# Optimization experiments

Hardware: AMD Instinct MI355X
Metric: run time of the kernel (lower is better)

The kernel has to match this reference:

```python
import jax, jax.numpy as jnp
import numpy as np

N_HEAD = 16
NEG = -1e30  # finite stand-in for -inf; keeps softmax NaN-free


def setup_inputs() -> dict:
    key = jax.random.key(0)
    k1, k2, k3, k4, k5, k6 = jax.random.split(key, 6)
    B, T, C = 4, 2048, 1024
    x = jax.random.normal(k1, (B, T, C), dtype=jnp.float32)
    # realistic right-padding: True = padded position
    lengths = jax.random.randint(k2, (B,), T // 2, T + 1)  # at least half valid
    padding_mask = jnp.arange(T)[None, :] >= lengths[:, None]  # [B,T] bool
    s = 0.02
    W_attn = jax.random.normal(k3, (C, 3 * C), dtype=jnp.float32) * s
    b_attn = jnp.zeros((3 * C,), dtype=jnp.float32)
    W_proj = jax.random.normal(k4, (C, C), dtype=jnp.float32) * s
    b_proj = jnp.zeros((C,), dtype=jnp.float32)
    return {"x": x, "padding_mask": padding_mask, "W_attn": W_attn,
            "b_attn": b_attn, "W_proj": W_proj, "b_proj": b_proj}


def reference(x, padding_mask, W_attn, b_attn, W_proj, b_proj):
    B, T, C = x.shape
    H, D = N_HEAD, C // N_HEAD
    qkv = x @ W_attn + b_attn  # [B,T,3C]
    q, k, v = jnp.split(qkv, 3, axis=-1)
    q = q.reshape(B, T, H, D).transpose(0, 2, 1, 3)  # [B,H,T,D]
    k = k.reshape(B, T, H, D).transpose(0, 2, 1, 3)
    v = v.reshape(B, T, H, D).transpose(0, 2, 1, 3)
    att = jnp.einsum('bhqd,bhkd->bhqk', q, k) / jnp.sqrt(jnp.float32(D))
    causal = jnp.tril(jnp.ones((T, T), dtype=bool))  # [T,T]
    invalid = padding_mask[:, None, None, :] | ~causal[None, None]  # [B,1,T,T] key invalid
    att = jnp.where(invalid, NEG, att)
    att = jax.nn.softmax(att, axis=-1)
    # rows where every key is masked: torch softmax gives NaN -> nan_to_num(0)
    any_valid = jnp.any(~invalid, axis=-1, keepdims=True)  # [B,1,T,1]
    att = jnp.where(any_valid, att, 0.0)
    y = jnp.einsum('bhqk,bhkd->bhqd', att, v)  # [B,H,T,D]
    y = y.transpose(0, 2, 1, 3).reshape(B, T, C)
    y = y @ W_proj + b_proj
    y = jnp.where(padding_mask[:, :, None], 0.0, y)
    return y
```

## Files before the change

kernel.cpp:

```cpp
#include <hip/hip_runtime.h>
#include <stdint.h>

#define T_SEQ 2048
#define CDIM  1024
#define NH    16
#define DH    64
#define BATCH 4
#define MROWS (BATCH * T_SEQ)
#define N3    (3 * CDIM)
#define NEGBIG -1e30f

typedef unsigned short u16;
typedef __attribute__((ext_vector_type(8))) __bf16 bf16x8;
typedef __attribute__((ext_vector_type(4))) __bf16 bf16x4;
typedef __attribute__((ext_vector_type(8))) unsigned short u16x8;
typedef __attribute__((ext_vector_type(4))) float f32x4;
typedef __attribute__((ext_vector_type(16))) float f32x16;
typedef __attribute__((ext_vector_type(4))) unsigned int u32x4;

__device__ inline u16 f2bf(float f) {
  uint32_t u = __builtin_bit_cast(uint32_t, f);
  u += 0x7FFFu + ((u >> 16) & 1u);
  return (u16)(u >> 16);
}

__device__ inline void gld_lds16(const void* g, void* l) {
  __builtin_amdgcn_global_load_lds(
      (const __attribute__((address_space(1))) void*)g,
      (__attribute__((address_space(3))) void*)l, 16, 0, 0);
}


__global__ __launch_bounds__(256) void cvt_f32_bf16(
    const float* __restrict__ in, u16* __restrict__ out, int n) {
  int i = (blockIdx.x * 256 + threadIdx.x) * 4;
  if (i >= n) return;
  float4 v = *(const float4*)&in[i];
  ushort4 o; o.x = f2bf(v.x); o.y = f2bf(v.y); o.z = f2bf(v.z); o.w = f2bf(v.w);
  *(ushort4*)&out[i] = o;
}

__global__ __launch_bounds__(256) void wt_tiled(
    const float* __restrict__ W, u16* __restrict__ WT, int K, int N) {
  __shared__ float tile[64][65];
  const int k0 = blockIdx.y * 64, n0 = blockIdx.x * 64;
  const int t = threadIdx.x, cr = t >> 6, cc = t & 63;
#pragma unroll
  for (int i = 0; i < 16; i++) {
    int r = i * 4 + cr;
    tile[r][cc] = W[(size_t)(k0 + r) * N + n0 + cc];
  }
  __syncthreads();
#pragma unroll
  for (int i = 0; i < 16; i++) {
    int r = i * 4 + cr;
    WT[(size_t)(n0 + r) * K + k0 + cc] = f2bf(tile[cc][r]);
  }
}

__global__ __launch_bounds__(256) void len_kernel(
    const void* __restrict__ maskp, int* __restrict__ lengths) {
  __shared__ int flag;
  __shared__ int red[256];
  const int t = threadIdx.x, b = blockIdx.x;
  if (t == 0) flag = 0;
  __syncthreads();
  const uint32_t* mw = (const uint32_t*)maskp;
  int f = 0;
  for (int i = t; i < 2048; i += 256) f |= (mw[i] > 1u) ? 1 : 0;
  if (f) atomicOr(&flag, 1);
  __syncthreads();
  int cnt = 0;
  if (flag) {
    const uint8_t* mb = (const uint8_t*)maskp;
    for (int i = t; i < T_SEQ; i += 256) cnt += (mb[(size_t)b * T_SEQ + i] == 0);
  } else {
    const int* mi = (const int*)maskp;
    for (int i = t; i < T_SEQ; i += 256) cnt += (mi[(size_t)b * T_SEQ + i] == 0);
  }
  red[t] = cnt;
  __syncthreads();
  for (int s = 128; s > 0; s >>= 1) {
    if (t < s) red[t] += red[t + s];
    __syncthreads();
  }
  if (t == 0) lengths[b] = red[0];
}

template <int MODE>
__global__ __launch_bounds__(256, 2) void gemm_bf16(
    const u16* __restrict__ A, const u16* __restrict__ Bt,
    const float* __restrict__ bias,
    u16* __restrict__ Qb, u16* __restrict__ Kb, u16* __restrict__ Vt,
    float* __restrict__ Out, const int* __restrict__ lengths,
    int Mdim, int Ndim, int Kdim) {
  __shared__ u16 SM[16384];
  u16* As = SM;
  u16* Bs = SM + 8192;
  const int t = threadIdx.x;
  const int lane = t & 63, wid = t >> 6;
  const int wr = wid >> 1, wc = wid & 1;
  const int r16 = lane & 15, kg = lane >> 4;
  const int m0 = blockIdx.y * 128, n0 = blockIdx.x * 128;
  const int bb = m0 >> 11, tt0 = m0 & 2047;

  if (tt0 >= lengths[bb]) {
    if (MODE == 1) {
      const float4 z4 = make_float4(0.f, 0.f, 0.f, 0.f);
#pragma unroll
      for (int i = 0; i < 16; i++) {
        int u = i * 256 + t;
        int r = u >> 5, c4 = u & 31;
        *(float4*)&Out[(size_t)(m0 + r) * CDIM + n0 + c4 * 4] = z4;
      }
    }
    return;
  }

  f32x4 acc[4][4];
#pragma unroll
  for (int i = 0; i < 4; i++)
#pragma unroll
    for (int j = 0; j < 4; j++) acc[i][j] = (f32x4){0.f, 0.f, 0.f, 0.f};

  for (int k0 = 0; k0 < Kdim; k0 += 64) {
#pragma unroll
    for (int i = 0; i < 4; i++) {
      int idx = i * 256 + t;
      int row = idx >> 3;
      int chunk = idx & 7;
      int colel = (chunk * 8) ^ ((row & 7) << 3);
      gld_lds16(&A[(size_t)(m0 + row) * Kdim + k0 + colel], &As[idx * 8]);
      gld_lds16(&Bt[(size_t)(n0 + row) * Kdim + k0 + colel], &Bs[idx * 8]);
    }
    __syncthreads();

#pragma unroll
    for (int s = 0; s < 2; s++) {
      bf16x8 af[4], bfr[4];
#pragma unroll
      for (int m = 0; m < 4; m++) {
        int row = wr * 64 + m * 16 + r16;
        int colel = (s * 32 + kg * 8) ^ ((row & 7) << 3);
        af[m] = *(const bf16x8*)&As[row * 64 + colel];
      }
#pragma unroll
      for (int n = 0; n < 4; n++) {
        int row = wc * 64 + n * 16 + r16;
        int colel = (s * 32 + kg * 8) ^ ((row & 7) << 3);
        bfr[n] = *(const bf16x8*)&Bs[row * 64 + colel];
      }
#pragma unroll
      for (int m = 0; m < 4; m++)
#pragma unroll
        for (int n = 0; n < 4; n++)
          acc[m][n] = __builtin_amdgcn_mfma_f32_16x16x32_bf16(
              af[m], bfr[n], acc[m][n], 0, 0, 0);
    }
    __syncthreads();
  }

  if (MODE == 0) {
    const int b = bb;
    if (n0 >= 2048) {
      u16* Tt = SM;
#pragma unroll
      for (int m = 0; m < 4; m++)
#pragma unroll
        for (int n = 0; n < 4; n++) {
          int ln = wc * 64 + n * 16 + r16;
          float bv = bias[n0 + ln];
#pragma unroll
          for (int reg = 0; reg < 4; reg++) {
            int lm = wr * 64 + m * 16 + kg * 4 + reg;
            Tt[ln * 128 + (lm ^ ((ln & 7) << 3))] = f2bf(acc[m][n][reg] + bv);
          }
        }
      __syncthreads();
      const int cbase = n0 - 2048;
#pragma unroll
      for (int i = 0; i < 8; i++) {
        int u = i * 256 + t;
        int ln = u >> 4, ch = u & 15;
        u16x8 v = *(const u16x8*)&Tt[ln * 128 + ((ch * 8) ^ ((ln & 7) << 3))];
        int c = cbase + ln, hh = c >> 6, d = c & 63;
        *(u16x8*)&Vt[(((size_t)b * NH + hh) * DH + d) * T_SEQ + tt0 + ch * 8] = v;
      }
    } else {
      u16* Tt = SM;
#pragma unroll
      for (int m = 0; m < 4; m++)
#pragma unroll
        for (int n = 0; n < 4; n++) {
          int ln = wc * 64 + n * 16 + r16;
          float bv = bias[n0 + ln];
#pragma unroll
          for (int reg = 0; reg < 4; reg++) {
            int lm = wr * 64 + m * 16 + kg * 4 + reg;
            Tt[lm * 128 + (ln ^ ((lm & 7) << 3))] = f2bf(acc[m][n][reg] + bv);
          }
        }
      __syncthreads();
      const int cb = n0 & 1023;
      u16* dst = (n0 < 1024) ? Qb : Kb;
#pragma unroll
      for (int i = 0; i < 8; i++) {
        int u = i * 256 + t;
        int row = u >> 4, ch = u & 15;
        u16x8 v = *(const u16x8*)&Tt[row * 128 + ((ch * 8) ^ ((row & 7) << 3))];
        int c = cb + ch * 8, hh = c >> 6, d = c & 63;
        *(u16x8*)&dst[((size_t)(b * NH + hh) * T_SEQ + tt0 + row) * DH + d] = v;
      }
    }
    return;
  }

#pragma unroll
  for (int m = 0; m < 4; m++) {
    int gmb = m0 + wr * 64 + m * 16 + kg * 4;
#pragma unroll
    for (int n = 0; n < 4; n++) {
      int gn = n0 + wc * 64 + n * 16 + r16;
      float bv = bias[gn];
#pragma unroll
      for (int reg = 0; reg < 4; reg++) {
        float v = acc[m][n][reg] + bv;
        int row = gmb + reg;
        int b = row >> 11, tt = row & 2047;
        if (tt >= lengths[b]) v = 0.f;
        Out[(size_t)row * CDIM + gn] = v;
      }
    }
  }
}

__global__ __launch_bounds__(256) void attn32p_kernel(
    const u16* __restrict__ Qb, const u16* __restrict__ Kb,
    const u16* __restrict__ Vt, u16* __restrict__ yb,
    const int* __restrict__ lengths) {
  __shared__ __attribute__((aligned(16))) char smem[65536];
  const int t = threadIdx.x, lane = t & 63, wid = t >> 6;
  const int l31 = lane & 31, hi = lane >> 5;
  const int bh = blockIdx.y, b = bh >> 4, h = bh & (NH - 1);
  const int len = lengths[b];
  const int nAct = (len + 127) >> 7;
  const int npairs = (nAct + 1) >> 1;
  const int iq = blockIdx.x;
  if (iq >= npairs) return;
  const int q0L = iq * 128;
  const int q0H = (nAct - 1 - iq) * 128;
  const bool hiAct = q0H > q0L;
  const int q0Lw = q0L + wid * 32, q0Hw = q0H + wid * 32;
  const int qrowL = q0Lw + l31, qrowH = q0Hw + l31;
  const u16* Qh = Qb + (size_t)bh * T_SEQ * DH;
  const u16* Kh = Kb + (size_t)bh * T_SEQ * DH;
  const u16* Vth = Vt + (size_t)bh * DH * T_SEQ;
  const float SC = 0.18033688011112042f;
  const float THR = 44.3614195558365f;

  const int lenceil = (len + 63) & ~63;
  const int kvH = (q0H + 128 < lenceil) ? q0H + 128 : lenceil;
  const int kvL = (q0L + 128 < lenceil) ? q0L + 128 : lenceil;
  const int kv_end = hiAct ? kvH : kvL;
  const int ntiles = kv_end >> 6;

  bf16x8 qfL[4], qfH[4];
#pragma unroll
  for (int ks = 0; ks < 4; ks++) {
    qfL[ks] = *(const bf16x8*)&Qh[(size_t)qrowL * DH + ks * 16 + hi * 8];
    qfH[ks] = *(const bf16x8*)&Qh[(size_t)qrowH * DH + ks * 16 + hi * 8];
  }

  f32x16 oaccL[2], oaccH[2];
  oaccL[0] = (f32x16)0.f; oaccL[1] = (f32x16)0.f;
  oaccH[0] = (f32x16)0.f; oaccH[1] = (f32x16)0.f;
  float mL = NEGBIG, lL = 0.f, mH = NEGBIG, lH = 0.f;

  const int idx0 = t, idx1 = 256 + t;
  const int row0 = idx0 >> 3, ch0 = idx0 & 7;
  const int row1 = idx1 >> 3, ch1 = idx1 & 7;
  const int kc0 = (ch0 * 8) ^ ((row0 & 7) << 3);
  const int kc1 = (ch1 * 8) ^ ((row1 & 7) << 3);
  const char* kp0 = (const char*)Kh + ((size_t)row0 * DH + kc0) * 2;
  const char* kp1 = (const char*)Kh + ((size_t)row1 * DH + kc1) * 2;
  const char* vp0 = (const char*)Vth + ((size_t)row0 * T_SEQ + kc0) * 2;
  const char* vp1 = (const char*)Vth + ((size_t)row1 * T_SEQ + kc1) * 2;

  auto STAGE = [&](int bsel) {
    char* base = smem + bsel * 16384;
    gld_lds16(kp0, base + idx0 * 16);
    gld_lds16(kp1, base + idx1 * 16);
    gld_lds16(vp0, base + 8192 + idx0 * 16);
    gld_lds16(vp1, base + 8192 + idx1 * 16);
    kp0 += 8192; kp1 += 8192; vp0 += 128; vp1 += 128;
  };

  auto FLASH = [&](const u16* Ks, const u16* Vts, int kv0, int q0w, int qrow,
                   bf16x8* qf, f32x16* oacc, float& mrun, float& lrun) {
    f32x16 sacc[2];
    sacc[0] = (f32x16)0.f; sacc[1] = (f32x16)0.f;
#pragma unroll
    for (int kb = 0; kb < 2; kb++)
#pragma unroll
      for (int ks = 0; ks < 4; ks++) {
        int row = kb * 32 + l31;
        int col = (ks * 16 + hi * 8) ^ ((row & 7) << 3);
        bf16x8 ak = *(const bf16x8*)&Ks[row * 64 + col];
        sacc[kb] = __builtin_amdgcn_mfma_f32_32x32x16_bf16(
            ak, qf[ks], sacc[kb], 0, 0, 0);
      }

    if ((kv0 + 63 > q0w) || (kv0 + 64 > len)) {
#pragma unroll
      for (int kb = 0; kb < 2; kb++)
#pragma unroll
        for (int r = 0; r < 16; r++) {
          int key = kv0 + kb * 32 + (r & 3) + 8 * (r >> 2) + 4 * hi;
          if (key > qrow || key >= len) sacc[kb][r] = NEGBIG;
        }
    }
    float tm[16];
#pragma unroll
    for (int r = 0; r < 16; r++) tm[r] = fmaxf(sacc[0][r], sacc[1][r]);
#pragma unroll
    for (int r = 0; r < 8; r++) tm[r] = fmaxf(tm[r], tm[r + 8]);
#pragma unroll
    for (int r = 0; r < 4; r++) tm[r] = fmaxf(tm[r], tm[r + 4]);
    tm[0] = fmaxf(fmaxf(tm[0], tm[2]), fmaxf(tm[1], tm[3]));

    if (!__all(tm[0] <= mrun + THR)) {
      float mt = fmaxf(tm[0], __shfl_xor(tm[0], 32));
      float mnew = fmaxf(mrun, mt);
      float fac = exp2f((mrun - mnew) * SC);
      mrun = mnew;
      lrun *= fac;
#pragma unroll
      for (int r = 0; r < 16; r++) { oacc[0][r] *= fac; oacc[1][r] *= fac; }
    }
    const float msc = mrun * SC;
#pragma unroll
    for (int kb = 0; kb < 2; kb++)
#pragma unroll
      for (int r = 0; r < 16; r++)
        sacc[kb][r] = exp2f(fmaf(sacc[kb][r], SC, -msc));
    float pt[16];
#pragma unroll
    for (int r = 0; r < 16; r++) pt[r] = sacc[0][r] + sacc[1][r];
#pragma unroll
    for (int r = 0; r < 8; r++) pt[r] += pt[r + 8];
#pragma unroll
    for (int r = 0; r < 4; r++) pt[r] += pt[r + 4];
    lrun += (pt[0] + pt[2]) + (pt[1] + pt[3]);

#pragma unroll
    for (int ks = 0; ks < 4; ks++) {
      const int kb = ks >> 1, rb = (ks & 1) * 8;
      uint32_t d0, d1, d2, d3;
      asm("v_cvt_pk_bf16_f32 %0, %1, %2" : "=v"(d0)
          : "v"(sacc[kb][rb + 0]), "v"(sacc[kb][rb + 1]));
      asm("v_cvt_pk_bf16_f32 %0, %1, %2" : "=v"(d1)
          : "v"(sacc[kb][rb + 2]), "v"(sacc[kb][rb + 3]));
      asm("v_cvt_pk_bf16_f32 %0, %1, %2" : "=v"(d2)
          : "v"(sacc[kb][rb + 4]), "v"(sacc[kb][rb + 5]));
      asm("v_cvt_pk_bf16_f32 %0, %1, %2" : "=v"(d3)
          : "v"(sacc[kb][rb + 6]), "v"(sacc[kb][rb + 7]));
      bf16x8 pb = __builtin_bit_cast(bf16x8, (u32x4){d0, d1, d2, d3});
#pragma unroll
      for (int mb = 0; mb < 2; mb++) {
        int row = mb * 32 + l31;
        int sw = (row & 7);
        bf16x4 v1 = *(const bf16x4*)&Vts[row * 64 + ((2 * ks) ^ sw) * 8 + 4 * hi];
        bf16x4 v2 = *(const bf16x4*)&Vts[row * 64 + ((2 * ks + 1) ^ sw) * 8 + 4 * hi];
        bf16x8 av;
#pragma unroll
        for (int j = 0; j < 4; j++) { av[j] = v1[j]; av[4 + j] = v2[j]; }
        oacc[mb] = __builtin_amdgcn_mfma_f32_32x32x16_bf16(
            av, pb, oacc[mb], 0, 0, 0);
      }
    }
  };

  STAGE(0); STAGE(1);
  for (int it = 0; it < ntiles; ++it) {
    if (it + 2 < ntiles) STAGE((it + 2) & 3);
    const int r = ntiles - 1 - it;
    if (r >= 2)      asm volatile("s_waitcnt vmcnt(8)" ::: "memory");
    else if (r == 1) asm volatile("s_waitcnt vmcnt(4)" ::: "memory");
    else             asm volatile("s_waitcnt vmcnt(0)" ::: "memory");
    __builtin_amdgcn_s_barrier();
    __builtin_amdgcn_sched_barrier(0);

    const u16* Ks  = (const u16*)(smem + (it & 3) * 16384);
    const u16* Vts = (const u16*)(smem + (it & 3) * 16384 + 8192);
    const int kv0 = it << 6;
    if (hiAct && kv0 <= q0Hw + 31)
      FLASH(Ks, Vts, kv0, q0Hw, qrowH, qfH, oaccH, mH, lH);
    if (kv0 <= q0Lw + 31)
      FLASH(Ks, Vts, kv0, q0Lw, qrowL, qfL, oaccL, mL, lL);
  }
  __syncthreads();

  u16* yt = (u16*)smem + wid * (32 * 72);
  auto EPI = [&](f32x16* oacc, float lrun, int q0w) {
    float lt = lrun + __shfl_xor(lrun, 32);
    const float inv = (lt > 0.f) ? 1.f / lt : 0.f;
#pragma unroll
    for (int mb = 0; mb < 2; mb++)
#pragma unroll
      for (int r = 0; r < 16; r += 2) {
        int d = mb * 32 + (r & 3) + 8 * (r >> 2) + 4 * hi;
        float a0 = oacc[mb][r] * inv, a1 = oacc[mb][r + 1] * inv;
        uint32_t pw;
        asm("v_cvt_pk_bf16_f32 %0, %1, %2" : "=v"(pw) : "v"(a0), "v"(a1));
        *(uint32_t*)&yt[l31 * 72 + d] = pw;
      }
    asm volatile("s_waitcnt lgkmcnt(0)" ::: "memory");
    __builtin_amdgcn_sched_barrier(0);
#pragma unroll
    for (int pass = 0; pass < 4; pass++) {
      int rowq = pass * 8 + (lane >> 3);
      int col8 = (lane & 7) * 8;
      u16x8 v = *(const u16x8*)&yt[rowq * 72 + col8];
      *(u16x8*)&yb[((size_t)b * T_SEQ + q0w + rowq) * CDIM + h * DH + col8] = v;
    }
    asm volatile("s_waitcnt lgkmcnt(0)" ::: "memory");
    __builtin_amdgcn_sched_barrier(0);
  };
  EPI(oaccL, lL, q0Lw);
  if (hiAct) EPI(oaccH, lH, q0Hw);
}

extern "C" void kernel_launch(void* const* d_in, const int* in_sizes, int n_in,
                              void* d_out, int out_size, void* d_ws, size_t ws_size,
                              hipStream_t stream) {
  const float* x  = (const float*)d_in[0];
  const void*  mask = d_in[1];
  const float* Wa = (const float*)d_in[2];
  const float* ba = (const float*)d_in[3];
  const float* Wp = (const float*)d_in[4];
  const float* bp = (const float*)d_in[5];
  float* out = (float*)d_out;

  char* w = (char*)d_ws;
  u16* xb  = (u16*)w; w += (size_t)MROWS * CDIM * 2;
  u16* WaT = (u16*)w; w += (size_t)N3 * CDIM * 2;
  u16* WpT = (u16*)w; w += (size_t)CDIM * CDIM * 2;
  u16* Qb  = (u16*)w; w += (size_t)MROWS * CDIM * 2;
  u16* Kb  = (u16*)w; w += (size_t)MROWS * CDIM * 2;
  u16* Vt  = (u16*)w; w += (size_t)MROWS * CDIM * 2;
  int* lengths = (int*)w;
  u16* yb = xb;

  cvt_f32_bf16<<<(MROWS * CDIM / 4 + 255) / 256, 256, 0, stream>>>(x, xb, MROWS * CDIM);
  wt_tiled<<<dim3(N3 / 64, CDIM / 64), 256, 0, stream>>>(Wa, WaT, CDIM, N3);
  wt_tiled<<<dim3(CDIM / 64, CDIM / 64), 256, 0, stream>>>(Wp, WpT, CDIM, CDIM);
  len_kernel<<<BATCH, 256, 0, stream>>>(mask, lengths);

  gemm_bf16<0><<<dim3(N3 / 128, MROWS / 128), 256, 0, stream>>>(
      xb, WaT, ba, Qb, Kb, Vt, nullptr, lengths, MROWS, N3, CDIM);

  attn32p_kernel<<<dim3(8, BATCH * NH), 256, 0, stream>>>(
      Qb, Kb, Vt, yb, lengths);

  gemm_bf16<1><<<dim3(CDIM / 128, MROWS / 128), 256, 0, stream>>>(
      yb, WpT, bp, nullptr, nullptr, nullptr, out, lengths, MROWS, CDIM, CDIM);
}
```

Before: 224.1 us.

## Process KV tiles in pairs, issuing both QK^T MFMAs before softmax

The flash-attention loop now handles two 64-key tiles per iteration. It issues the QK^T MFMAs for both tiles before doing softmax and PV for each, so matrix work can overlap the softmax ALU work. Staging now loads two tiles per chunk, and the wait is a full vmcnt(0) plus barrier per chunk. The cost is higher register pressure from holding two score accumulators, and less fine-grained prefetch overlap, since the 4-slot ring is now effectively double-buffered per chunk.

```diff
diff --git a/kernel.cpp b/kernel.cpp
--- a/kernel.cpp
+++ b/kernel.cpp
@@ -295,9 +295,7 @@
     kp0 += 8192; kp1 += 8192; vp0 += 128; vp1 += 128;
   };
 
-  auto FLASH = [&](const u16* Ks, const u16* Vts, int kv0, int q0w, int qrow,
-                   bf16x8* qf, f32x16* oacc, float& mrun, float& lrun) {
-    f32x16 sacc[2];
+  auto QKT = [&](const u16* Ks, bf16x8* qf, f32x16* sacc) {
     sacc[0] = (f32x16)0.f; sacc[1] = (f32x16)0.f;
 #pragma unroll
     for (int kb = 0; kb < 2; kb++)
@@ -309,7 +307,10 @@
         sacc[kb] = __builtin_amdgcn_mfma_f32_32x32x16_bf16(
             ak, qf[ks], sacc[kb], 0, 0, 0);
       }
-
+  };
+
+  auto SMPV = [&](f32x16* sacc, const u16* Vts, int kv0, int q0w, int qrow,
+                  f32x16* oacc, float& mrun, float& lrun) {
     if ((kv0 + 63 > q0w) || (kv0 + 64 > len)) {
 #pragma unroll
       for (int kb = 0; kb < 2; kb++)
@@ -381,22 +382,40 @@
   };
 
   STAGE(0); STAGE(1);
-  for (int it = 0; it < ntiles; ++it) {
-    if (it + 2 < ntiles) STAGE((it + 2) & 3);
-    const int r = ntiles - 1 - it;
-    if (r >= 2)      asm volatile("s_waitcnt vmcnt(8)" ::: "memory");
-    else if (r == 1) asm volatile("s_waitcnt vmcnt(4)" ::: "memory");
-    else             asm volatile("s_waitcnt vmcnt(0)" ::: "memory");
+  const int nchunks = (ntiles + 1) >> 1;
+  for (int c = 0; c < nchunks; ++c) {
+    asm volatile("s_waitcnt vmcnt(0)" ::: "memory");
     __builtin_amdgcn_s_barrier();
     __builtin_amdgcn_sched_barrier(0);
-
-    const u16* Ks  = (const u16*)(smem + (it & 3) * 16384);
-    const u16* Vts = (const u16*)(smem + (it & 3) * 16384 + 8192);
-    const int kv0 = it << 6;
-    if (hiAct && kv0 <= q0Hw + 31)
-      FLASH(Ks, Vts, kv0, q0Hw, qrowH, qfH, oaccH, mH, lH);
-    if (kv0 <= q0Lw + 31)
-      FLASH(Ks, Vts, kv0, q0Lw, qrowL, qfL, oaccL, mL, lL);
+    if (c + 1 < nchunks) {
+      STAGE((2 * c + 2) & 3);
+      STAGE((2 * c + 3) & 3);
+    }
+
+    const int t0 = 2 * c, t1 = 2 * c + 1;
+    const int kv0 = t0 << 6, kv1 = t1 << 6;
+    const u16* Ks0  = (const u16*)(smem + (t0 & 3) * 16384);
+    const u16* Vts0 = (const u16*)(smem + (t0 & 3) * 16384 + 8192);
+    const u16* Ks1  = (const u16*)(smem + (t1 & 3) * 16384);
+    const u16* Vts1 = (const u16*)(smem + (t1 & 3) * 16384 + 8192);
+    const bool t1v = t1 < ntiles;
+
+    if (hiAct && kv0 <= q0Hw + 31) {
+      const bool two = t1v && (kv1 <= q0Hw + 31);
+      f32x16 s0[2], s1[2];
+      QKT(Ks0, qfH, s0);
+      if (two) QKT(Ks1, qfH, s1);
+      SMPV(s0, Vts0, kv0, q0Hw, qrowH, oaccH, mH, lH);
+      if (two) SMPV(s1, Vts1, kv1, q0Hw, qrowH, oaccH, mH, lH);
+    }
+    if (kv0 <= q0Lw + 31) {
+      const bool two = t1v && (kv1 <= q0Lw + 31);
+      f32x16 s0[2], s1[2];
+      QKT(Ks0, qfL, s0);
+      if (two) QKT(Ks1, qfL, s1);
+      SMPV(s0, Vts0, kv0, q0Lw, qrowL, oaccL, mL, lL);
+      if (two) SMPV(s1, Vts1, kv1, q0Lw, qrowL, oaccL, mL, lL);
+    }
   }
   __syncthreads();
 
```

Result: faster. 218.1 us, median of 2 (-2.7%).
